# Kernel tuning notes

Measured on AMD Instinct MI355X. Metric: run time of the kernel, lower is better.

## Reference

```python
import jax, jax.numpy as jnp
import numpy as np

INPUT_DIM = 128
HIDDEN_DIM = 512
STACK_DIM = 64
BATCH = 128
MAX_T = 259  # 2*128 + 3
SEQ_L = 259  # l, so k = (l-3)//2 = 128


def setup_inputs() -> dict:
    key = jax.random.key(0)
    ks = jax.random.split(key, 7)
    G = 4 * HIDDEN_DIM
    x = jax.random.normal(ks[0], (SEQ_L, BATCH, INPUT_DIM), dtype=jnp.float32)
    Wih = jax.random.normal(ks[1], (G, INPUT_DIM + STACK_DIM), dtype=jnp.float32) * 0.05
    bih = jax.random.normal(ks[2], (G,), dtype=jnp.float32) * 0.05
    Whh = jax.random.normal(ks[3], (G, HIDDEN_DIM), dtype=jnp.float32) * 0.05
    bhh = jax.random.normal(ks[4], (G,), dtype=jnp.float32) * 0.05
    Wr = jax.random.normal(ks[5], (INPUT_DIM + STACK_DIM + 2, HIDDEN_DIM), dtype=jnp.float32) * 0.05
    br = jax.random.normal(ks[6], (INPUT_DIM + STACK_DIM + 2,), dtype=jnp.float32) * 0.05
    return {"x": x, "Wih": Wih, "bih": bih, "Whh": Whh, "bhh": bhh, "Wr": Wr, "br": br}


def _forward(x, Wih, bih, Whh, bhh, Wr, br):
    l = x.shape[0]
    k = (l - 3) // 2
    B = x.shape[1]

    def lstm_cell(xin, h, c):
        # torch.nn.LSTMCell: gate order i, f, g, o
        g = xin @ Wih.T + bih + h @ Whh.T + bhh  # [B, 4H]
        i, f, gg, o = jnp.split(g, 4, axis=1)
        c2 = jax.nn.sigmoid(f) * c + jax.nn.sigmoid(i) * jnp.tanh(gg)
        h2 = jax.nn.sigmoid(o) * jnp.tanh(c2)
        return h2, c2

    def update_stack(V, s, vt, ut, dt, t):
        Vp = V.at[:, t, :].add(vt)  # scatter vt into row t (row was zero)
        # baddbmm with strict-upper-triangular ones matrix == suffix sum:
        # prod[b, i] = sum_{j > i} s[b, j]
        prod = jnp.cumsum(s[:, ::-1], axis=1)[:, ::-1] - s
        sp = jnp.maximum(0.0, s - jnp.maximum(0.0, ut - prod))
        sp = sp.at[:, t].set(dt[:, 0])
        inner = jax.nn.relu(1.0 - prod - sp)  # uses prod from OLD s, as in source
        A = jnp.minimum(sp, inner)  # [B, MAX_T]
        rt = jnp.einsum('bt,btd->bd', A, Vp)
        return Vp, sp, rt

    def step(carry, inp):
        V, s, h, c, rt = carry
        xt, t = inp
        h, c = lstm_cell(jnp.concatenate([xt, rt], axis=1), h, c)
        out = h @ Wr.T + br  # [B, S + I + 2]
        vt = out[:, :STACK_DIM]
        ot = out[:, STACK_DIM:STACK_DIM + INPUT_DIM]
        ut = jax.nn.sigmoid(out[:, STACK_DIM + INPUT_DIM:STACK_DIM + INPUT_DIM + 1])
        dt = jax.nn.sigmoid(out[:, STACK_DIM + INPUT_DIM + 1:])
        V, s, rt = update_stack(V, s, vt, ut, dt, t)
        return (V, s, h, c, rt), ot

    dt_ = x.dtype
    carry = (jnp.zeros((B, MAX_T, STACK_DIM), dt_),
             jnp.zeros((B, MAX_T), dt_),
             jnp.zeros((B, HIDDEN_DIM), dt_),
             jnp.zeros((B, HIDDEN_DIM), dt_),
             jnp.zeros((B, STACK_DIM), dt_))
    # encode phase: steps 0..k with real inputs (outputs discarded)
    carry, _ = jax.lax.scan(step, carry, (x[:k + 1], jnp.arange(k + 1)))
    # decode phase: steps k+1..2k+2 with zero inputs (same encode_LSTM, per source)
    xz = jnp.zeros((k + 2, B, INPUT_DIM), dt_)
    carry, ots = jax.lax.scan(step, carry, (xz, k + 1 + jnp.arange(k + 2)))
    return jax.nn.log_softmax(ots, axis=2)  # [k+2, B, INPUT_DIM]


def reference(x, Wih, bih, Whh, bhh, Wr, br):
    return _forward(x, Wih, bih, Whh, bhh, Wr, br)
```

## Files before the change

kernel.cpp:

```cpp
#include <hip/hip_runtime.h>
#include <hip/hip_bf16.h>
#include <math.h>

#define IDIM 128
#define HDIM 512
#define SDIM 64
#define BATCH 128
#define MAXT 259
#define G4 2048
#define KTOT 704
#define ROUT 194
#define AFRAG_U 73728
#define NBLK 256
#define NGATE 16
#define PJ 224
#define PTJ 224

typedef __hip_bfloat16 bf16;
typedef __attribute__((ext_vector_type(8))) short short8;
typedef __attribute__((ext_vector_type(4))) float floatx4;

__device__ __forceinline__ float sigmoidf_(float v) { return 1.f / (1.f + expf(-v)); }
__device__ __forceinline__ float b2f(bf16 v) { return __bfloat162float(v); }
__device__ __forceinline__ float load_in(const void* p, size_t i, int isf32) {
    return isf32 ? ((const float*)p)[i] : b2f(((const bf16*)p)[i]);
}
__device__ __forceinline__ unsigned short f2bfbits(float v) {
    unsigned u = __builtin_bit_cast(unsigned, v);
    unsigned r = (u + 0x7FFFu + ((u >> 16) & 1u)) >> 16;
    return (unsigned short)r;
}
__device__ __forceinline__ float bfbits2f(unsigned short b) {
    return __builtin_bit_cast(float, (unsigned)b << 16);
}
__device__ __forceinline__ unsigned aload(const unsigned* p) {
    return __hip_atomic_load(p, __ATOMIC_RELAXED, __HIP_MEMORY_SCOPE_AGENT);
}
__device__ __forceinline__ unsigned long long aload64(const unsigned long long* p) {
    return __hip_atomic_load(p, __ATOMIC_RELAXED, __HIP_MEMORY_SCOPE_AGENT);
}
__device__ __forceinline__ void astore64(unsigned long long* p, unsigned long long v) {
    __hip_atomic_store(p, v, __ATOMIC_RELAXED, __HIP_MEMORY_SCOPE_AGENT);
}
__device__ __forceinline__ unsigned long long packf2(float a, float b) {
    return (unsigned long long)__builtin_bit_cast(unsigned, a)
         | ((unsigned long long)__builtin_bit_cast(unsigned, b) << 32);
}
__device__ __forceinline__ void unpack_frag(const unsigned long long* ap,
                                            short8& ah, short8& al) {
    #pragma unroll
    for (int j = 0; j < 4; j++) {
        unsigned long long q = aload64(ap + j);
        unsigned u0 = (unsigned)q, u1 = (unsigned)(q >> 32);
        ah[2 * j]     = (short)(u0 & 0xffffu);
        al[2 * j]     = (short)(u0 >> 16);
        ah[2 * j + 1] = (short)(u1 & 0xffffu);
        al[2 * j + 1] = (short)(u1 >> 16);
    }
}

__device__ __forceinline__ void wait_flags16(const unsigned* f, int base16,
                                             unsigned tgt) {
    if (threadIdx.x < 16) {
        while (aload(&f[(base16 + (int)threadIdx.x) * 16]) < tgt)
            __builtin_amdgcn_s_sleep(1);
    }
    __atomic_signal_fence(__ATOMIC_SEQ_CST);
    __syncthreads();
}

__global__ void detect_kernel(const unsigned short* __restrict__ w, int* __restrict__ flag) {
    if (threadIdx.x == 0) {
        int isf32 = 0;
        for (int i = 0; i < 256; i++) {
            int e = (w[i] >> 7) & 0xFF;
            if (e >= 0x8F) isf32 = 1;
        }
        *flag = isf32;
    }
}

__global__ void prep_kernel(const void* __restrict__ Wih, const void* __restrict__ bih,
                            const void* __restrict__ Whh, const void* __restrict__ bhh,
                            unsigned short* __restrict__ WfH, unsigned short* __restrict__ WfL,
                            float* __restrict__ bc, const int* __restrict__ flag) {
    int isf32 = *flag;
    int jp = blockIdx.x;
    int u = jp >> 2, gate = jp & 3;
    int src = gate * HDIM + u;
    int jt = jp >> 4, jn = jp & 15;
    for (int k = threadIdx.x; k < KTOT; k += blockDim.x) {
        float v = (k < 192) ? load_in(Wih, (size_t)src * 192 + k, isf32)
                            : load_in(Whh, (size_t)src * HDIM + (k - 192), isf32);
        unsigned short hi = f2bfbits(v);
        unsigned short lo = f2bfbits(v - bfbits2f(hi));
        int ks = k >> 5, q = (k & 31) >> 3, e = k & 7;
        size_t d = (((size_t)jt * 22 + ks) * 64 + (q * 16 + jn)) * 8 + e;
        WfH[d] = hi;
        WfL[d] = lo;
    }
    if (threadIdx.x == 0)
        bc[jp] = load_in(bih, src, isf32) + load_in(bhh, src, isf32);
}

__global__ void wr_prep_kernel(const void* __restrict__ Wr, const void* __restrict__ br,
                               unsigned short* __restrict__ WrBh, unsigned short* __restrict__ WrBl,
                               float* __restrict__ brf, const int* __restrict__ flag) {
    int isf32 = *flag;
    int j = blockIdx.x;
    for (int k = threadIdx.x; k < HDIM; k += blockDim.x) {
        float v = (j < ROUT) ? load_in(Wr, (size_t)j * HDIM + k, isf32) : 0.f;
        unsigned short hi = f2bfbits(v);
        WrBh[(size_t)j * HDIM + k] = hi;
        WrBl[(size_t)j * HDIM + k] = f2bfbits(v - bfbits2f(hi));
    }
    if (threadIdx.x == 0) brf[j] = (j < ROUT) ? load_in(br, j, isf32) : 0.f;
}

__global__ __launch_bounds__(256) void persist_kernel(
        const void* __restrict__ x,
        const unsigned short* __restrict__ WfH, const unsigned short* __restrict__ WfL,
        const float* __restrict__ bc,
        const unsigned short* __restrict__ WrBh, const unsigned short* __restrict__ WrBl,
        const float* __restrict__ brf,
        unsigned* __restrict__ AfP,
        float* __restrict__ part,
        unsigned short* __restrict__ Vg,
        void* __restrict__ dout, const int* __restrict__ flag,
        unsigned* __restrict__ hfl, unsigned* __restrict__ pfl,
        unsigned* __restrict__ rtf) {
    __shared__ __align__(16) short Ahs[18 * 64 * 8];
    __shared__ __align__(16) short Als[18 * 64 * 8];
    __shared__ __align__(16) unsigned short wrslB[14 * 64 * 8];
    __shared__ __align__(16) unsigned short wrslBL[14 * 64 * 8];
    __shared__ __align__(16) float scr[8][16][20];
    __shared__ __align__(16) unsigned short hlh[16 * 40];
    __shared__ __align__(16) unsigned short hll[16 * 40];
    __shared__ __align__(16) float outs[208];
    __shared__ __align__(16) float sL[324];
    __shared__ __align__(16) float aL[324];
    __shared__ __align__(16) float red[4][64];
    __shared__ __align__(16) float brS[208];
    __shared__ __align__(16) float bcS[128];
    __shared__ int e0S;

    const int tid = threadIdx.x, lane = tid & 63, wv = tid >> 6;
    const int blk = blockIdx.x, ms = blk >> 5, ns = blk & 31;
    const int isf32 = *flag;
    float* const pt = (float*)Ahs;

    const int is_gate = (ns < 16);
    const int gb = ns;
    const int pb = ns - 16;
    const int p2row = ms * 16 + pb;

    if (is_gate) {
        for (int i = tid; i < 14 * 64 * 8; i += 256) {
            int jt = i >> 9, l = (i >> 3) & 63, e = i & 7;
            size_t src = (size_t)(jt * 16 + (l & 15)) * HDIM + gb * 32 + (l >> 4) * 8 + e;
            wrslB[i]  = WrBh[src];
            wrslBL[i] = WrBl[src];
        }
        if (tid < 128) bcS[tid] = bc[gb * 128 + tid];
    } else {
        for (int i = tid; i < 208; i += 256) brS[i] = brf[i];
        for (int i = tid; i < 324; i += 256) { sL[i] = 0.f; aL[i] = 0.f; }
    }
    __syncthreads();

    if (is_gate) {
        const short8* WH = (const short8*)WfH;
        const short8* WL = (const short8*)WfL;
        const int jt0 = gb * 8 + wv, jt1 = gb * 8 + 4 + wv;
        const short8* wb0  = WH + (size_t)jt0 * 22 * 64;
        const short8* wb1  = WH + (size_t)jt1 * 22 * 64;
        const short8* wbl0 = WL + (size_t)jt0 * 22 * 64;
        const short8* wbl1 = WL + (size_t)jt1 * 22 * 64;
        float cc0 = 0.f, cc1 = 0.f;

        for (int t = 0; t < MAXT; t++) {
            const int cur = t & 1, nxt = cur ^ 1;
            const unsigned long long* AfPc64 =
                (const unsigned long long*)(AfP + (size_t)cur * AFRAG_U);
            unsigned long long* AfPn64 =
                (unsigned long long*)(AfP + (size_t)nxt * AFRAG_U);
            const int use_x = (t < 129);

            wait_flags16(hfl, ms * 16, (unsigned)t);

            #pragma unroll
            for (int i0 = 0; i0 < 4; i0++) {
                int i = i0 * 256 + tid;
                int ksi = 2 + (i >> 6), l = i & 63;
                const unsigned long long* ap =
                    AfPc64 + ((size_t)(ms * 18 + ksi) * 64 + l) * 4;
                short8 ah, al8;
                unpack_frag(ap, ah, al8);
                *(short8*)&Ahs[(ksi * 64 + l) * 8] = ah;
                *(short8*)&Als[(ksi * 64 + l) * 8] = al8;
            }
            __syncthreads();

            floatx4 acc0 = {0.f, 0.f, 0.f, 0.f};
            floatx4 acc1 = {0.f, 0.f, 0.f, 0.f};
            if (use_x) {
                int m = lane & 15, q = lane >> 4;
                size_t xrow = ((size_t)t * BATCH + ms * 16 + m) * IDIM + q * 8;
                #pragma unroll
                for (int ks = 0; ks < 4; ks++) {
                    short8 a;
                    if (isf32) {
                        const float* xf = (const float*)x + xrow + ks * 32;
                        #pragma unroll
                        for (int i = 0; i < 8; i++) a[i] = (short)f2bfbits(xf[i]);
                    } else {
                        a = *(const short8*)((const unsigned short*)x + xrow + ks * 32);
                    }
                    acc0 = __builtin_amdgcn_mfma_f32_16x16x32_bf16(a, wb0[ks * 64 + lane], acc0, 0, 0, 0);
                    acc1 = __builtin_amdgcn_mfma_f32_16x16x32_bf16(a, wb1[ks * 64 + lane], acc1, 0, 0, 0);
                    if (isf32) {
                        acc0 = __builtin_amdgcn_mfma_f32_16x16x32_bf16(a, wbl0[ks * 64 + lane], acc0, 0, 0, 0);
                        acc1 = __builtin_amdgcn_mfma_f32_16x16x32_bf16(a, wbl1[ks * 64 + lane], acc1, 0, 0, 0);
                    }
                }
            }
            #pragma unroll 4
            for (int ksi = 2; ksi < 18; ksi++) {
                int ks = 4 + ksi;
                short8 ah  = *(const short8*)&Ahs[(ksi * 64 + lane) * 8];
                short8 al8 = *(const short8*)&Als[(ksi * 64 + lane) * 8];
                short8 bh0 = wb0[ks * 64 + lane];
                short8 bh1 = wb1[ks * 64 + lane];
                acc0 = __builtin_amdgcn_mfma_f32_16x16x32_bf16(ah, bh0, acc0, 0, 0, 0);
                acc0 = __builtin_amdgcn_mfma_f32_16x16x32_bf16(al8, bh0, acc0, 0, 0, 0);
                acc1 = __builtin_amdgcn_mfma_f32_16x16x32_bf16(ah, bh1, acc1, 0, 0, 0);
                acc1 = __builtin_amdgcn_mfma_f32_16x16x32_bf16(al8, bh1, acc1, 0, 0, 0);
                if (isf32) {
                    acc0 = __builtin_amdgcn_mfma_f32_16x16x32_bf16(ah, wbl0[ks * 64 + lane], acc0, 0, 0, 0);
                    acc1 = __builtin_amdgcn_mfma_f32_16x16x32_bf16(ah, wbl1[ks * 64 + lane], acc1, 0, 0, 0);
                }
            }

            wait_flags16(rtf, ms * 16, (unsigned)t);

            if (tid < 128) {
                int ksi = tid >> 6, l = tid & 63;
                const unsigned long long* ap =
                    AfPc64 + ((size_t)(ms * 18 + ksi) * 64 + l) * 4;
                short8 ah, al8;
                unpack_frag(ap, ah, al8);
                *(short8*)&Ahs[(ksi * 64 + l) * 8] = ah;
                *(short8*)&Als[(ksi * 64 + l) * 8] = al8;
            }
            __syncthreads();
            #pragma unroll
            for (int ksi = 0; ksi < 2; ksi++) {
                int ks = 4 + ksi;
                short8 ah  = *(const short8*)&Ahs[(ksi * 64 + lane) * 8];
                short8 al8 = *(const short8*)&Als[(ksi * 64 + lane) * 8];
                short8 bh0 = wb0[ks * 64 + lane];
                short8 bh1 = wb1[ks * 64 + lane];
                acc0 = __builtin_amdgcn_mfma_f32_16x16x32_bf16(ah, bh0, acc0, 0, 0, 0);
                acc0 = __builtin_amdgcn_mfma_f32_16x16x32_bf16(al8, bh0, acc0, 0, 0, 0);
                acc1 = __builtin_amdgcn_mfma_f32_16x16x32_bf16(ah, bh1, acc1, 0, 0, 0);
                acc1 = __builtin_amdgcn_mfma_f32_16x16x32_bf16(al8, bh1, acc1, 0, 0, 0);
                if (isf32) {
                    acc0 = __builtin_amdgcn_mfma_f32_16x16x32_bf16(ah, wbl0[ks * 64 + lane], acc0, 0, 0, 0);
                    acc1 = __builtin_amdgcn_mfma_f32_16x16x32_bf16(ah, wbl1[ks * 64 + lane], acc1, 0, 0, 0);
                }
            }
            {
                int n = lane & 15, m0 = (lane >> 4) * 4;
                #pragma unroll
                for (int r = 0; r < 4; r++) scr[wv][m0 + r][n] = acc0[r];
                #pragma unroll
                for (int r = 0; r < 4; r++) scr[wv + 4][m0 + r][n] = acc1[r];
            }
            __syncthreads();
            {
                int r = tid >> 4, p = tid & 15;
                float4 g = *(const float4*)&scr[p >> 2][r][(p & 3) * 4];
                float4 bb = *(const float4*)&bcS[p * 4];
                float c2 = sigmoidf_(g.y + bb.y) * cc0 + sigmoidf_(g.x + bb.x) * tanhf(g.z + bb.z);
                float h2 = sigmoidf_(g.w + bb.w) * tanhf(c2);
                cc0 = c2;
                unsigned short hi0 = f2bfbits(h2);
                hlh[r * 40 + p] = hi0;
                hll[r * 40 + p] = f2bfbits(h2 - bfbits2f(hi0));
                int u1 = p + 16;
                float4 g1 = *(const float4*)&scr[u1 >> 2][r][(u1 & 3) * 4];
                float4 bb1 = *(const float4*)&bcS[u1 * 4];
                float c21 = sigmoidf_(g1.y + bb1.y) * cc1 + sigmoidf_(g1.x + bb1.x) * tanhf(g1.z + bb1.z);
                float h21 = sigmoidf_(g1.w + bb1.w) * tanhf(c21);
                cc1 = c21;
                unsigned short hi1 = f2bfbits(h21);
                hlh[r * 40 + u1] = hi1;
                hll[r * 40 + u1] = f2bfbits(h21 - bfbits2f(hi1));
            }
            __syncthreads();
            {
                int rr = tid >> 4, pp = tid & 15;
                unsigned short hb0 = hlh[rr * 40 + 2 * pp];
                unsigned short lb0 = hll[rr * 40 + 2 * pp];
                unsigned short hb1 = hlh[rr * 40 + 2 * pp + 1];
                unsigned short lb1 = hll[rr * 40 + 2 * pp + 1];
                unsigned u0 = (unsigned)hb0 | ((unsigned)lb0 << 16);
                unsigned u1 = (unsigned)hb1 | ((unsigned)lb1 << 16);
                int u_g = gb * 32 + 2 * pp;
                int ksi2 = 2 + (u_g >> 5), q = (u_g & 31) >> 3, e = u_g & 7;
                size_t fi = (((size_t)ms * 18 + ksi2) * 64 + q * 16 + rr) * 8 + e;
                astore64(AfPn64 + fi / 2, (unsigned long long)u0 | ((unsigned long long)u1 << 32));
            }
            asm volatile("s_waitcnt vmcnt(0)" ::: "memory");
            __syncthreads();
            if (tid == 0)
                __hip_atomic_store(&hfl[(ms * 16 + gb) * 16], (unsigned)(t + 1),
                                   __ATOMIC_RELAXED, __HIP_MEMORY_SCOPE_AGENT);

            {
                int m = lane & 15, q = lane >> 4;
                short8 ahh = *(const short8*)&hlh[m * 40 + q * 8];
                short8 ahl = *(const short8*)&hll[m * 40 + q * 8];
                int n = lane & 15, m0 = (lane >> 4) * 4;
                for (int jt = wv; jt < 14; jt += 4) {
                    const short8* bB  = (const short8*)&wrslB[((size_t)jt * 64 + lane) * 8];
                    const short8* bBl = (const short8*)&wrslBL[((size_t)jt * 64 + lane) * 8];
                    floatx4 accR = {0.f, 0.f, 0.f, 0.f};
                    short8 bh = *bB;
                    accR = __builtin_amdgcn_mfma_f32_16x16x32_bf16(ahh, bh, accR, 0, 0, 0);
                    accR = __builtin_amdgcn_mfma_f32_16x16x32_bf16(ahl, bh, accR, 0, 0, 0);
                    if (isf32) {
                        short8 bl = *bBl;
                        accR = __builtin_amdgcn_mfma_f32_16x16x32_bf16(ahh, bl, accR, 0, 0, 0);
                        accR = __builtin_amdgcn_mfma_f32_16x16x32_bf16(ahl, bl, accR, 0, 0, 0);
                    }
                    #pragma unroll
                    for (int ri = 0; ri < 4; ri++)
                        pt[(m0 + ri) * PTJ + jt * 16 + n] = accR[ri];
                }
            }
            __syncthreads();
            {
                #pragma unroll
                for (int it = 0; it < 4; it++) {
                    int rloc = wv * 4 + it;
                    int prow_ = ms * 16 + rloc;
                    const float* pr = pt + rloc * PTJ;
                    unsigned long long* pb64 =
                        (unsigned long long*)(part + (((size_t)prow_ * NGATE) + gb) * PJ);
                    if (use_x) {
                        if (lane < 32)
                            astore64(pb64 + lane, packf2(pr[2 * lane], pr[2 * lane + 1]));
                        else if (lane < 42) {
                            int l2 = lane - 32;
                            astore64(pb64 + 96 + l2,
                                     packf2(pr[192 + 2 * l2], pr[193 + 2 * l2]));
                        }
                    } else {
                        astore64(pb64 + lane, packf2(pr[2 * lane], pr[2 * lane + 1]));
                        if (lane < 40)
                            astore64(pb64 + 64 + lane,
                                     packf2(pr[128 + 2 * lane], pr[129 + 2 * lane]));
                    }
                }
            }
            asm volatile("s_waitcnt vmcnt(0)" ::: "memory");
            __syncthreads();
            if (tid == 0)
                __hip_atomic_store(&pfl[(ms * 16 + gb) * 16], (unsigned)(t + 1),
                                   __ATOMIC_RELAXED, __HIP_MEMORY_SCOPE_AGENT);
        }
    } else {
        unsigned short* Vrow = Vg + (size_t)p2row * MAXT * SDIM;
        for (int t = 0; t < MAXT; t++) {
            unsigned long long* AfPn64 =
                (unsigned long long*)(AfP + (size_t)((t + 1) & 1) * AFRAG_U);

            wait_flags16(pfl, ms * 16, (unsigned)(t + 1));

            if (tid < 208) {
                const unsigned* pb2 = (const unsigned*)part
                                    + (size_t)p2row * NGATE * PJ + tid;
                float s4 = brS[tid];
                #pragma unroll
                for (int g = 0; g < NGATE; g++)
                    s4 += __builtin_bit_cast(float, aload(pb2 + (size_t)g * PJ));
                outs[tid] = s4;
            }
            __syncthreads();
            if (wv == 0) {
                float uval = sigmoidf_(outs[192]);
                float dval = sigmoidf_(outs[193]);
                Vrow[t * SDIM + lane] = f2bfbits(outs[lane]);
                int ebase = lane * 5;
                float sv[5], suf[5];
                #pragma unroll
                for (int j = 0; j < 5; j++) {
                    int e = ebase + j;
                    sv[j] = (e < MAXT) ? sL[e] : 0.f;
                }
                suf[4] = sv[4];
                #pragma unroll
                for (int j = 3; j >= 0; j--) suf[j] = sv[j] + suf[j + 1];
                float ltot = suf[0];
                float accs = ltot;
                #pragma unroll
                for (int off = 1; off < 64; off <<= 1) {
                    float y = __shfl_down(accs, off, 64);
                    if (lane + off < 64) accs += y;
                }
                float after_lane = accs - ltot;
                int emin = 0x7fffffff;
                #pragma unroll
                for (int j = 0; j < 5; j++) {
                    int e = ebase + j;
                    if (e <= t) {
                        float prod = after_lane + (suf[j] - sv[j]);
                        float sp = (e == t) ? dval
                                            : fmaxf(0.f, sv[j] - fmaxf(0.f, uval - prod));
                        float inner = fmaxf(0.f, 1.f - prod - sp);
                        sL[e] = sp;
                        aL[e] = fminf(sp, inner);
                        if (prod < 1.f && e < emin) emin = e;
                    }
                }
                #pragma unroll
                for (int off = 32; off; off >>= 1) {
                    int o = __shfl_xor(emin, off, 64);
                    emin = o < emin ? o : emin;
                }
                if (lane == 0) e0S = emin;
            }
            __syncthreads();
            {
                const int e0 = e0S;
                float racc = 0.f;
                if (e0 <= t) {
                    int i2s = e0 + ((wv - e0) & 3);
                    for (int i2 = i2s; i2 <= t; i2 += 4)
                        racc += aL[i2] * bfbits2f(Vrow[i2 * SDIM + lane]);
                }
                red[wv][lane] = racc;
            }
            __syncthreads();
            if (wv == 0) {
                float rtv = red[0][lane] + red[1][lane] + red[2][lane] + red[3][lane];
                float rtn = __shfl_down(rtv, 1, 64);
                if ((lane & 1) == 0) {
                    unsigned short hb0 = f2bfbits(rtv);
                    unsigned short lb0 = f2bfbits(rtv - bfbits2f(hb0));
                    unsigned short hb1 = f2bfbits(rtn);
                    unsigned short lb1 = f2bfbits(rtn - bfbits2f(hb1));
                    unsigned u0 = (unsigned)hb0 | ((unsigned)lb0 << 16);
                    unsigned u1 = (unsigned)hb1 | ((unsigned)lb1 << 16);
                    int d0 = lane;
                    int ksi = d0 >> 5, q = (d0 & 31) >> 3, e = d0 & 7;
                    size_t fi = (((size_t)ms * 18 + ksi) * 64 + q * 16 + pb) * 8 + e;
                    astore64(AfPn64 + fi / 2,
                             (unsigned long long)u0 | ((unsigned long long)u1 << 32));
                }
                asm volatile("s_waitcnt vmcnt(0)" ::: "memory");
                if (lane == 0)
                    __hip_atomic_store(&rtf[(ms * 16 + pb) * 16], (unsigned)(t + 1),
                                       __ATOMIC_RELAXED, __HIP_MEMORY_SCOPE_AGENT);
            } else if (wv == 1 && t >= 129) {
                float a = outs[64 + lane];
                float bvv = outs[128 + lane];
                float m = fmaxf(a, bvv);
                #pragma unroll
                for (int off = 32; off; off >>= 1) m = fmaxf(m, __shfl_xor(m, off, 64));
                float e = expf(a - m) + expf(bvv - m);
                #pragma unroll
                for (int off = 32; off; off >>= 1) e += __shfl_xor(e, off, 64);
                float ls = logf(e) + m;
                size_t base = ((size_t)(t - 129) * BATCH + p2row) * IDIM;
                if (isf32) {
                    ((float*)dout)[base + lane] = a - ls;
                    ((float*)dout)[base + lane + 64] = bvv - ls;
                } else {
                    ((bf16*)dout)[base + lane] = __float2bfloat16(a - ls);
                    ((bf16*)dout)[base + lane + 64] = __float2bfloat16(bvv - ls);
                }
            }
        }
    }
}

extern "C" void kernel_launch(void* const* d_in, const int* in_sizes, int n_in,
                              void* d_out, int out_size, void* d_ws, size_t ws_size,
                              hipStream_t stream) {
    const void* x   = d_in[0];
    const void* Wih = d_in[1];
    const void* bih = d_in[2];
    const void* Whh = d_in[3];
    const void* bhh = d_in[4];
    const void* Wr  = d_in[5];
    const void* br  = d_in[6];

    char* base = (char*)d_ws;
    size_t off = 0;
    int* flag = (int*)base;                                   off += 64;
    unsigned* hfl = (unsigned*)(base + off);                  off += 128 * 64 + 64;
    unsigned* pfl = (unsigned*)(base + off);                  off += 128 * 64 + 64;
    unsigned* rtf = (unsigned*)(base + off);                  off += 128 * 64 + 64;
    unsigned short* WfH  = (unsigned short*)(base + off);     off += (size_t)G4 * KTOT * 2;
    unsigned short* WfL  = (unsigned short*)(base + off);     off += (size_t)G4 * KTOT * 2;
    unsigned short* WrBh = (unsigned short*)(base + off);     off += (size_t)224 * HDIM * 2;
    unsigned short* WrBl = (unsigned short*)(base + off);     off += (size_t)224 * HDIM * 2;
    float* bc   = (float*)(base + off);                       off += G4 * 4;
    float* brf  = (float*)(base + off);                       off += 1024;
    unsigned* AfP = (unsigned*)(base + off);                  size_t af_off = off;
                                                              off += (size_t)2 * AFRAG_U * 4;
    float* part = (float*)(base + off);                       off += (size_t)BATCH * NGATE * PJ * 4;
    unsigned short* Vg = (unsigned short*)(base + off);       off += (size_t)BATCH * MAXT * SDIM * 2;

    hipMemsetAsync(base + 64, 0, 3 * (128 * 64 + 64), stream);
    hipMemsetAsync(base + af_off, 0, (size_t)2 * AFRAG_U * 4, stream);
    hipMemsetAsync(part, 0, (size_t)BATCH * NGATE * PJ * 4, stream);

    detect_kernel<<<1, 64, 0, stream>>>((const unsigned short*)Wih, flag);
    prep_kernel<<<G4, 256, 0, stream>>>(Wih, bih, Whh, bhh, WfH, WfL, bc, flag);
    wr_prep_kernel<<<224, 256, 0, stream>>>(Wr, br, WrBh, WrBl, brf, flag);

    persist_kernel<<<NBLK, 256, 0, stream>>>(x, WfH, WfL, bc, WrBh, WrBl, brf,
                                             AfP, part, Vg, d_out, flag,
                                             hfl, pfl, rtf);

    (void)in_sizes; (void)n_in; (void)out_size; (void)ws_size;
}
```

Before: 3.012 ms.

## Split readout partials into critical stack part and deferred output part

Gate blocks now compute only the stack-critical readout columns (vt, ut, dt) before signalling the stack blocks. The ot/log-softmax columns are computed afterward into a double-buffered partO with their own flag, which takes them off the recurrent critical path. The x-input MFMA contribution is also hoisted before the wait on the h flag so it overlaps with waiting. The cost is an extra flag set, a second partial buffer and more synchronisation in the decode phase.

Measured after the change: 3.075 ms. 1.02x slower.

```diff
diff --git a/kernel.cpp b/kernel.cpp
--- a/kernel.cpp
+++ b/kernel.cpp
@@ -13,8 +13,9 @@
 #define AFRAG_U 73728
 #define NBLK 256
 #define NGATE 16
-#define PJ 224
 #define PTJ 224
+#define PCJ 80
+#define POJ 128
 
 typedef __hip_bfloat16 bf16;
 typedef __attribute__((ext_vector_type(8))) short short8;
@@ -124,11 +125,12 @@
         const unsigned short* __restrict__ WrBh, const unsigned short* __restrict__ WrBl,
         const float* __restrict__ brf,
         unsigned* __restrict__ AfP,
-        float* __restrict__ part,
+        float* __restrict__ partC,
+        float* __restrict__ partO,
         unsigned short* __restrict__ Vg,
         void* __restrict__ dout, const int* __restrict__ flag,
         unsigned* __restrict__ hfl, unsigned* __restrict__ pfl,
-        unsigned* __restrict__ rtf) {
+        unsigned* __restrict__ rtf, unsigned* __restrict__ oflg) {
     __shared__ __align__(16) short Ahs[18 * 64 * 8];
     __shared__ __align__(16) short Als[18 * 64 * 8];
     __shared__ __align__(16) unsigned short wrslB[14 * 64 * 8];
@@ -136,10 +138,12 @@
     __shared__ __align__(16) float scr[8][16][20];
     __shared__ __align__(16) unsigned short hlh[16 * 40];
     __shared__ __align__(16) unsigned short hll[16 * 40];
-    __shared__ __align__(16) float outs[208];
+    __shared__ __align__(16) float outsC[80];
     __shared__ __align__(16) float sL[324];
     __shared__ __align__(16) float aL[324];
     __shared__ __align__(16) float red[4][64];
+    __shared__ __align__(16) float redo[128][2];
+    __shared__ __align__(16) float oL[128];
     __shared__ __align__(16) float brS[208];
     __shared__ __align__(16) float bcS[128];
     __shared__ int e0S;
@@ -186,8 +190,31 @@
                 (unsigned long long*)(AfP + (size_t)nxt * AFRAG_U);
             const int use_x = (t < 129);
 
+            floatx4 acc0 = {0.f, 0.f, 0.f, 0.f};
+            floatx4 acc1 = {0.f, 0.f, 0.f, 0.f};
+            if (use_x) {
+                int m = lane & 15, q = lane >> 4;
+                size_t xrow = ((size_t)t * BATCH + ms * 16 + m) * IDIM + q * 8;
+                #pragma unroll
+                for (int ks = 0; ks < 4; ks++) {
+                    short8 a;
+                    if (isf32) {
+                        const float* xf = (const float*)x + xrow + ks * 32;
+                        #pragma unroll
+                        for (int i = 0; i < 8; i++) a[i] = (short)f2bfbits(xf[i]);
+                    } else {
+                        a = *(const short8*)((const unsigned short*)x + xrow + ks * 32);
+                    }
+                    acc0 = __builtin_amdgcn_mfma_f32_16x16x32_bf16(a, wb0[ks * 64 + lane], acc0, 0, 0, 0);
+                    acc1 = __builtin_amdgcn_mfma_f32_16x16x32_bf16(a, wb1[ks * 64 + lane], acc1, 0, 0, 0);
+                    if (isf32) {
+                        acc0 = __builtin_amdgcn_mfma_f32_16x16x32_bf16(a, wbl0[ks * 64 + lane], acc0, 0, 0, 0);
+                        acc1 = __builtin_amdgcn_mfma_f32_16x16x32_bf16(a, wbl1[ks * 64 + lane], acc1, 0, 0, 0);
+                    }
+                }
+            }
+
             wait_flags16(hfl, ms * 16, (unsigned)t);
-
             #pragma unroll
             for (int i0 = 0; i0 < 4; i0++) {
                 int i = i0 * 256 + tid;
@@ -201,29 +228,6 @@
             }
             __syncthreads();
 
-            floatx4 acc0 = {0.f, 0.f, 0.f, 0.f};
-            floatx4 acc1 = {0.f, 0.f, 0.f, 0.f};
-            if (use_x) {
-                int m = lane & 15, q = lane >> 4;
-                size_t xrow = ((size_t)t * BATCH + ms * 16 + m) * IDIM + q * 8;
-                #pragma unroll
-                for (int ks = 0; ks < 4; ks++) {
-                    short8 a;
-                    if (isf32) {
-                        const float* xf = (const float*)x + xrow + ks * 32;
-                        #pragma unroll
-                        for (int i = 0; i < 8; i++) a[i] = (short)f2bfbits(xf[i]);
-                    } else {
-                        a = *(const short8*)((const unsigned short*)x + xrow + ks * 32);
-                    }
-                    acc0 = __builtin_amdgcn_mfma_f32_16x16x32_bf16(a, wb0[ks * 64 + lane], acc0, 0, 0, 0);
-                    acc1 = __builtin_amdgcn_mfma_f32_16x16x32_bf16(a, wb1[ks * 64 + lane], acc1, 0, 0, 0);
-                    if (isf32) {
-                        acc0 = __builtin_amdgcn_mfma_f32_16x16x32_bf16(a, wbl0[ks * 64 + lane], acc0, 0, 0, 0);
-                        acc1 = __builtin_amdgcn_mfma_f32_16x16x32_bf16(a, wbl1[ks * 64 + lane], acc1, 0, 0, 0);
-                    }
-                }
-            }
             #pragma unroll 4
             for (int ksi = 2; ksi < 18; ksi++) {
                 int ks = 4 + ksi;
@@ -242,7 +246,6 @@
             }
 
             wait_flags16(rtf, ms * 16, (unsigned)t);
-
             if (tid < 128) {
                 int ksi = tid >> 6, l = tid & 63;
                 const unsigned long long* ap =
@@ -322,7 +325,10 @@
                 short8 ahh = *(const short8*)&hlh[m * 40 + q * 8];
                 short8 ahl = *(const short8*)&hll[m * 40 + q * 8];
                 int n = lane & 15, m0 = (lane >> 4) * 4;
-                for (int jt = wv; jt < 14; jt += 4) {
+                #pragma unroll
+                for (int sel = 0; sel < 2; sel++) {
+                    int jt = sel == 0 ? wv : 12;
+                    if (sel == 1 && wv != 0) break;
                     const short8* bB  = (const short8*)&wrslB[((size_t)jt * 64 + lane) * 8];
                     const short8* bBl = (const short8*)&wrslBL[((size_t)jt * 64 + lane) * 8];
                     floatx4 accR = {0.f, 0.f, 0.f, 0.f};
@@ -347,21 +353,11 @@
                     int prow_ = ms * 16 + rloc;
                     const float* pr = pt + rloc * PTJ;
                     unsigned long long* pb64 =
-                        (unsigned long long*)(part + (((size_t)prow_ * NGATE) + gb) * PJ);
-                    if (use_x) {
-                        if (lane < 32)
-                            astore64(pb64 + lane, packf2(pr[2 * lane], pr[2 * lane + 1]));
-                        else if (lane < 42) {
-                            int l2 = lane - 32;
-                            astore64(pb64 + 96 + l2,
-                                     packf2(pr[192 + 2 * l2], pr[193 + 2 * l2]));
-                        }
-                    } else {
+                        (unsigned long long*)(partC + (((size_t)prow_ * NGATE) + gb) * PCJ);
+                    if (lane < 32)
                         astore64(pb64 + lane, packf2(pr[2 * lane], pr[2 * lane + 1]));
-                        if (lane < 40)
-                            astore64(pb64 + 64 + lane,
-                                     packf2(pr[128 + 2 * lane], pr[129 + 2 * lane]));
-                    }
+                    else if (lane == 32)
+                        astore64(pb64 + 32, packf2(pr[192], pr[193]));
                 }
             }
             asm volatile("s_waitcnt vmcnt(0)" ::: "memory");
@@ -369,6 +365,50 @@
             if (tid == 0)
                 __hip_atomic_store(&pfl[(ms * 16 + gb) * 16], (unsigned)(t + 1),
                                    __ATOMIC_RELAXED, __HIP_MEMORY_SCOPE_AGENT);
+
+            if (!use_x) {
+                {
+                    int m = lane & 15, q = lane >> 4;
+                    short8 ahh = *(const short8*)&hlh[m * 40 + q * 8];
+                    short8 ahl = *(const short8*)&hll[m * 40 + q * 8];
+                    int n = lane & 15, m0 = (lane >> 4) * 4;
+                    #pragma unroll
+                    for (int s2 = 0; s2 < 2; s2++) {
+                        int jt = 4 + wv + s2 * 4;
+                        const short8* bB  = (const short8*)&wrslB[((size_t)jt * 64 + lane) * 8];
+                        const short8* bBl = (const short8*)&wrslBL[((size_t)jt * 64 + lane) * 8];
+                        floatx4 accR = {0.f, 0.f, 0.f, 0.f};
+                        short8 bh = *bB;
+                        accR = __builtin_amdgcn_mfma_f32_16x16x32_bf16(ahh, bh, accR, 0, 0, 0);
+                        accR = __builtin_amdgcn_mfma_f32_16x16x32_bf16(ahl, bh, accR, 0, 0, 0);
+                        if (isf32) {
+                            short8 bl = *bBl;
+                            accR = __builtin_amdgcn_mfma_f32_16x16x32_bf16(ahh, bl, accR, 0, 0, 0);
+                            accR = __builtin_amdgcn_mfma_f32_16x16x32_bf16(ahl, bl, accR, 0, 0, 0);
+                        }
+                        #pragma unroll
+                        for (int ri = 0; ri < 4; ri++)
+                            pt[(m0 + ri) * PTJ + jt * 16 + n] = accR[ri];
+                    }
+                }
+                __syncthreads();
+                {
+                    #pragma unroll
+                    for (int it = 0; it < 4; it++) {
+                        int rloc = wv * 4 + it;
+                        int prow_ = ms * 16 + rloc;
+                        const float* pr = pt + rloc * PTJ;
+                        unsigned long long* pb64 = (unsigned long long*)
+                            (partO + ((((size_t)cur * BATCH + prow_) * NGATE) + gb) * POJ);
+                        astore64(pb64 + lane, packf2(pr[64 + 2 * lane], pr[65 + 2 * lane]));
+                    }
+                }
+                asm volatile("s_waitcnt vmcnt(0)" ::: "memory");
+                __syncthreads();
+                if (tid == 0)
+                    __hip_atomic_store(&oflg[(ms * 16 + gb) * 16], (unsigned)(t + 1),
+                                       __ATOMIC_RELAXED, __HIP_MEMORY_SCOPE_AGENT);
+            }
         }
     } else {
         unsigned short* Vrow = Vg + (size_t)p2row * MAXT * SDIM;
@@ -378,20 +418,20 @@
 
             wait_flags16(pfl, ms * 16, (unsigned)(t + 1));
 
-            if (tid < 208) {
-                const unsigned* pb2 = (const unsigned*)part
-                                    + (size_t)p2row * NGATE * PJ + tid;
-                float s4 = brS[tid];
+            if (tid < 66) {
+                const unsigned* pb2 = (const unsigned*)partC
+                                    + (size_t)p2row * NGATE * PCJ + tid;
+                float s4 = (tid < 64) ? brS[tid] : brS[128 + tid];
                 #pragma unroll
                 for (int g = 0; g < NGATE; g++)
-                    s4 += __builtin_bit_cast(float, aload(pb2 + (size_t)g * PJ));
-                outs[tid] = s4;
+                    s4 += __builtin_bit_cast(float, aload(pb2 + (size_t)g * PCJ));
+                outsC[tid] = s4;
             }
             __syncthreads();
             if (wv == 0) {
-                float uval = sigmoidf_(outs[192]);
-                float dval = sigmoidf_(outs[193]);
-                Vrow[t * SDIM + lane] = f2bfbits(outs[lane]);
+                float uval = sigmoidf_(outsC[64]);
+                float dval = sigmoidf_(outsC[65]);
+                Vrow[t * SDIM + lane] = f2bfbits(outsC[lane]);
                 int ebase = lane * 5;
                 float sv[5], suf[5];
                 #pragma unroll
@@ -463,23 +503,41 @@
                 if (lane == 0)
                     __hip_atomic_store(&rtf[(ms * 16 + pb) * 16], (unsigned)(t + 1),
                                        __ATOMIC_RELAXED, __HIP_MEMORY_SCOPE_AGENT);
-            } else if (wv == 1 && t >= 129) {
-                float a = outs[64 + lane];
-                float bvv = outs[128 + lane];
-                float m = fmaxf(a, bvv);
-                #pragma unroll
-                for (int off = 32; off; off >>= 1) m = fmaxf(m, __shfl_xor(m, off, 64));
-                float e = expf(a - m) + expf(bvv - m);
-                #pragma unroll
-                for (int off = 32; off; off >>= 1) e += __shfl_xor(e, off, 64);
-                float ls = logf(e) + m;
-                size_t base = ((size_t)(t - 129) * BATCH + p2row) * IDIM;
-                if (isf32) {
-                    ((float*)dout)[base + lane] = a - ls;
-                    ((float*)dout)[base + lane + 64] = bvv - ls;
-                } else {
-                    ((bf16*)dout)[base + lane] = __float2bfloat16(a - ls);
-                    ((bf16*)dout)[base + lane + 64] = __float2bfloat16(bvv - ls);
+            }
+            if (t >= 129) {
+                wait_flags16(oflg, ms * 16, (unsigned)(t + 1));
+                {
+                    int col = tid >> 1, half = tid & 1;
+                    const unsigned* pbo = (const unsigned*)partO
+                        + (((size_t)(t & 1) * BATCH + p2row) * NGATE) * POJ + col;
+                    float s = 0.f;
+                    #pragma unroll
+                    for (int g = 0; g < 8; g++)
+                        s += __builtin_bit_cast(float,
+                                aload(pbo + (size_t)(half * 8 + g) * POJ));
+                    redo[col][half] = s;
+                }
+                __syncthreads();
+                if (tid < 128) oL[tid] = redo[tid][0] + redo[tid][1] + brS[64 + tid];
+                __syncthreads();
+                if (wv == 0) {
+                    float a = oL[lane];
+                    float bvv = oL[64 + lane];
+                    float m = fmaxf(a, bvv);
+                    #pragma unroll
+                    for (int off = 32; off; off >>= 1) m = fmaxf(m, __shfl_xor(m, off, 64));
+                    float e = expf(a - m) + expf(bvv - m);
+                    #pragma unroll
+                    for (int off = 32; off; off >>= 1) e += __shfl_xor(e, off, 64);
+                    float ls = logf(e) + m;
+                    size_t base = ((size_t)(t - 129) * BATCH + p2row) * IDIM;
+                    if (isf32) {
+                        ((float*)dout)[base + lane] = a - ls;
+                        ((float*)dout)[base + lane + 64] = bvv - ls;
+                    } else {
+                        ((bf16*)dout)[base + lane] = __float2bfloat16(a - ls);
+                        ((bf16*)dout)[base + lane + 64] = __float2bfloat16(bvv - ls);
+                    }
                 }
             }
         }
@@ -503,6 +561,7 @@
     unsigned* hfl = (unsigned*)(base + off);                  off += 128 * 64 + 64;
     unsigned* pfl = (unsigned*)(base + off);                  off += 128 * 64 + 64;
     unsigned* rtf = (unsigned*)(base + off);                  off += 128 * 64 + 64;
+    unsigned* oflg = (unsigned*)(base + off);                 off += 128 * 64 + 64;
     unsigned short* WfH  = (unsigned short*)(base + off);     off += (size_t)G4 * KTOT * 2;
     unsigned short* WfL  = (unsigned short*)(base + off);     off += (size_t)G4 * KTOT * 2;
     unsigned short* WrBh = (unsigned short*)(base + off);     off += (size_t)224 * HDIM * 2;
@@ -511,20 +570,21 @@
     float* brf  = (float*)(base + off);                       off += 1024;
     unsigned* AfP = (unsigned*)(base + off);                  size_t af_off = off;
                                                               off += (size_t)2 * AFRAG_U * 4;
-    float* part = (float*)(base + off);                       off += (size_t)BATCH * NGATE * PJ * 4;
+    float* partC = (float*)(base + off);                      off += (size_t)BATCH * NGATE * PCJ * 4;
+    float* partO = (float*)(base + off);                      off += (size_t)2 * BATCH * NGATE * POJ * 4;
     unsigned short* Vg = (unsigned short*)(base + off);       off += (size_t)BATCH * MAXT * SDIM * 2;
 
-    hipMemsetAsync(base + 64, 0, 3 * (128 * 64 + 64), stream);
+    hipMemsetAsync(base + 64, 0, 4 * (128 * 64 + 64), stream);
     hipMemsetAsync(base + af_off, 0, (size_t)2 * AFRAG_U * 4, stream);
-    hipMemsetAsync(part, 0, (size_t)BATCH * NGATE * PJ * 4, stream);
+    hipMemsetAsync(partC, 0, (size_t)BATCH * NGATE * PCJ * 4, stream);
 
     detect_kernel<<<1, 64, 0, stream>>>((const unsigned short*)Wih, flag);
     prep_kernel<<<G4, 256, 0, stream>>>(Wih, bih, Whh, bhh, WfH, WfL, bc, flag);
     wr_prep_kernel<<<224, 256, 0, stream>>>(Wr, br, WrBh, WrBl, brf, flag);
 
     persist_kernel<<<NBLK, 256, 0, stream>>>(x, WfH, WfL, bc, WrBh, WrBl, brf,
-                                             AfP, part, Vg, d_out, flag,
-                                             hfl, pfl, rtf);
+                                             AfP, partC, partO, Vg, d_out, flag,
+                                             hfl, pfl, rtf, oflg);
 
     (void)in_sizes; (void)n_in; (void)out_size; (void)ws_size;
 }
```
